# Kernel optimization log

Measured on AMD Instinct MI355X. Metric: run time of the kernel, lower is better.

## Reference

```python
import jax, jax.numpy as jnp
import numpy as np

B = 32768
DIM = 768          # emb dim
NA = 1024          # outer n_anchors
K = 8              # n_comp (= n_patches P in relays)
PD = 16            # patch_dim
RD = K * PD        # relay_dim = 128
L = 2              # n_layers (relays)
RA = 16            # anchors per patch inside RelayLayer
NPH = 3            # n_phases
TD = NPH * RA      # tri_dim = 48
H = 64             # pw_hidden
MAG_MIN, MAG_MAX = 0.1, 5.0


def _nrm(x, eps=1e-12):
    return x / jnp.maximum(jnp.linalg.norm(x, axis=-1, keepdims=True), eps)


def _ln(x, g, b, eps=1e-5):
    mu = jnp.mean(x, axis=-1, keepdims=True)
    var = jnp.mean(jnp.square(x - mu), axis=-1, keepdims=True)
    return (x - mu) * jax.lax.rsqrt(var + eps) * g + b


def setup_inputs() -> dict:
    key = jax.random.key(0)
    ks = jax.random.split(key, 16)
    xav = lambda k, shp, fan_in, fan_out: jax.random.normal(k, shp, jnp.float32) * np.sqrt(2.0 / (fan_in + fan_out))
    home = _nrm(jax.random.normal(ks[3], (L, K, RA, PD), jnp.float32))
    anchors = _nrm(home + 0.05 * jax.random.normal(ks[4], (L, K, RA, PD), jnp.float32))
    return {
        'emb': jax.random.normal(ks[0], (B, DIM), jnp.float32),
        'triangulation': jax.random.normal(ks[1], (B, NA), jnp.float32),
        'raw_magnitude': jax.random.uniform(ks[2], (B, 1), jnp.float32),
        'emb_w': xav(ks[5], (DIM, RD // 2), DIM, RD // 2), 'emb_b': jnp.zeros((RD // 2,), jnp.float32),
        'tri_w': xav(ks[6], (NA, RD // 4), NA, RD // 4), 'tri_b': jnp.zeros((RD // 4,), jnp.float32),
        'ctx_w': xav(ks[7], (RD // 2 + RD // 4 + 1, RD), RD // 2 + RD // 4 + 1, RD), 'ctx_b': jnp.zeros((RD,), jnp.float32),
        'home': home, 'anchors': anchors,
        'pw_w1': xav(ks[8], (L, K, TD, H), TD, H), 'pw_b1': jnp.zeros((L, K, H), jnp.float32),
        'pw_w2': xav(ks[9], (L, K, H, PD), H, PD), 'pw_b2': jnp.zeros((L, K, PD), jnp.float32),
        'pwn_g': jnp.ones((L, PD), jnp.float32), 'pwn_b': jnp.zeros((L, PD), jnp.float32),
        'gates': jnp.full((L, K), -3.0, jnp.float32),
        'norm_g': jnp.ones((L, RD), jnp.float32), 'norm_b': jnp.zeros((L, RD), jnp.float32),
        'head_w1': xav(ks[10], (K, PD, PD // 2), PD, PD // 2), 'head_b1': jnp.zeros((K, PD // 2), jnp.float32),
        'head_w2': xav(ks[11], (K, PD // 2, 1), PD // 2, 1), 'head_b2': jnp.zeros((K, 1), jnp.float32),
        'stats_bias': jnp.zeros((K,), jnp.float32),
    }


def _relay(x, home, anchors, w1, b1, w2, b2, pg, pb, gates, ng, nb):
    Bb = x.shape[0]
    patches = _ln(x, ng, nb).reshape(Bb, K, PD)          # [B,P,d]
    pn = _nrm(patches)
    h = _nrm(home)                                       # [P,A,d]
    c = _nrm(anchors)
    cosw = jnp.clip(jnp.sum(h * c, axis=-1), -1 + 1e-7, 1 - 1e-7)
    omega = jnp.arccos(cosw)[..., None]                  # [P,A,1]
    so = jnp.maximum(jnp.sin(omega), 1e-7)
    tris = []
    for t in (0.0, 1.0 / 3.0, 2.0 / 3.0):
        at = _nrm((jnp.sin((1.0 - t) * omega) * h + jnp.sin(t * omega) * c) / so)
        tris.append(1.0 - jnp.einsum('bpd,pad->bpa', pn, at))
    tri = jnp.concatenate(tris, axis=-1)                 # [B,P,3A]
    hh = jax.nn.gelu(jnp.einsum('bpt,pth->bph', tri, w1) + b1, approximate=False)
    pw = _ln(jnp.einsum('bph,phd->bpd', hh, w2) + b2, pg, pb)
    g = jax.nn.sigmoid(gates)[None, :, None]             # [1,P,1]
    return x + (g * pw + (1.0 - g) * patches).reshape(Bb, -1)


def reference(emb, triangulation, raw_magnitude, emb_w, emb_b, tri_w, tri_b, ctx_w, ctx_b,
              home, anchors, pw_w1, pw_b1, pw_w2, pw_b2, pwn_g, pwn_b, gates, norm_g, norm_b,
              head_w1, head_b1, head_w2, head_b2, stats_bias):
    ctx = jnp.concatenate([emb @ emb_w + emb_b, triangulation @ tri_w + tri_b, raw_magnitude], axis=-1)
    x = ctx @ ctx_w + ctx_b                              # [B, RD]
    for l in range(L):
        x = _relay(x, home[l], anchors[l], pw_w1[l], pw_b1[l], pw_w2[l], pw_b2[l],
                   pwn_g[l], pwn_b[l], gates[l], norm_g[l], norm_b[l])
    patches = x.reshape(-1, K, PD)
    h1 = jax.nn.gelu(jnp.einsum('bkd,kdh->bkh', patches, head_w1) + head_b1, approximate=False)
    mc_raw = (jnp.einsum('bkh,kho->bko', h1, head_w2) + head_b2)[..., 0]   # [B,K]
    mc = MAG_MIN + (MAG_MAX - MAG_MIN) * jax.nn.sigmoid(mc_raw + stats_bias)
    mag = jnp.repeat(mc, NA // K, axis=-1)               # [B, NA]
    return (mag, mc)
```

## Files before the change

### kernel.cpp

```cpp
#include <hip/hip_runtime.h>
#include <hip/hip_bf16.h>
#include <math.h>

#define BTOT 32768

typedef float f32x4 __attribute__((ext_vector_type(4)));
typedef __bf16 v8bf __attribute__((ext_vector_type(8)));

__device__ float g_x[BTOT * 128];
__device__ float g_M[2 * 8 * 16 * 64];
__device__ float g_b1p[2 * 8 * 64];
__device__ __align__(16) unsigned short g_wf[1792 * 128];
__device__ float g_beff[128];
__device__ float g_wr[128];

__device__ __forceinline__ float fast_rcp(float x) {
#if __has_builtin(__builtin_amdgcn_rcpf)
    return __builtin_amdgcn_rcpf(x);
#else
    return 1.f / x;
#endif
}

__device__ __forceinline__ float gelu_f(float v) {
    const float p = v * fmaf(v * v, 0.0713548162f, 1.59576912f);
    return v * fast_rcp(1.f + __expf(-p));
}

__device__ __forceinline__ float fast_sigmoid(float v) {
    return fast_rcp(1.f + __expf(-v));
}

__device__ __forceinline__ unsigned short f2bf_rne(float x) {
    unsigned u = __float_as_uint(x);
    u += 0x7fffu + ((u >> 16) & 1u);
    return (unsigned short)(u >> 16);
}

#define GLOAD16(gp, lp)                                                        \
    __builtin_amdgcn_global_load_lds(                                          \
        (const __attribute__((address_space(1))) void*)(gp),                   \
        (__attribute__((address_space(3))) void*)(lp), 16, 0, 0)

__global__ __launch_bounds__(64) void k_pre(const float* __restrict__ home,
                                            const float* __restrict__ anchors,
                                            const float* __restrict__ pw_w1,
                                            const float* __restrict__ pw_b1) {
    __shared__ float s_AT[48 * 16];
    const int lp = blockIdx.x;
    const int tid = threadIdx.x;
    if (tid < 48) {
        const int t = tid >> 4, a = tid & 15;
        const float* hp = home + (lp * 16 + a) * 16;
        const float* cp = anchors + (lp * 16 + a) * 16;
        float h[16], c[16], nh = 0.f, nc = 0.f;
#pragma unroll
        for (int i = 0; i < 16; ++i) {
            h[i] = hp[i]; nh = fmaf(h[i], h[i], nh);
            c[i] = cp[i]; nc = fmaf(c[i], c[i], nc);
        }
        const float ih = 1.f / fmaxf(sqrtf(nh), 1e-12f);
        const float ic = 1.f / fmaxf(sqrtf(nc), 1e-12f);
        float cw = 0.f;
#pragma unroll
        for (int i = 0; i < 16; ++i) { h[i] *= ih; c[i] *= ic; cw = fmaf(h[i], c[i], cw); }
        cw = fminf(fmaxf(cw, -1.f + 1e-7f), 1.f - 1e-7f);
        const float om = acosf(cw);
        const float so = fmaxf(sinf(om), 1e-7f);
        const float tt = (float)t * (1.f / 3.f);
        const float s1 = sinf((1.f - tt) * om), s2 = sinf(tt * om);
        float v[16], nv = 0.f;
#pragma unroll
        for (int i = 0; i < 16; ++i) { v[i] = (s1 * h[i] + s2 * c[i]) / so; nv = fmaf(v[i], v[i], nv); }
        const float iv = 1.f / fmaxf(sqrtf(nv), 1e-12f);
#pragma unroll
        for (int i = 0; i < 16; ++i) s_AT[tid * 16 + i] = v[i] * iv;
    }
    __syncthreads();
    const int h = tid;
    const float* w1 = pw_w1 + lp * 48 * 64;
    float b = pw_b1[lp * 64 + h];
    float m[16];
#pragma unroll
    for (int d = 0; d < 16; ++d) m[d] = 0.f;
    for (int j = 0; j < 48; ++j) {
        const float w = w1[j * 64 + h];
        b += w;
#pragma unroll
        for (int d = 0; d < 16; ++d) m[d] = fmaf(s_AT[j * 16 + d], w, m[d]);
    }
    g_b1p[lp * 64 + h] = b;
#pragma unroll
    for (int d = 0; d < 16; ++d) g_M[(lp * 16 + d) * 64 + h] = m[d];
}

__global__ __launch_bounds__(256) void k_fold(const float* __restrict__ emb_w,
                                              const float* __restrict__ tri_w,
                                              const float* __restrict__ ctx_w,
                                              const float* __restrict__ ctx_b,
                                              const float* __restrict__ emb_b,
                                              const float* __restrict__ tri_b) {
    if (blockIdx.x == 56) {
        const int n = threadIdx.x;
        if (n < 128) {
            float b = ctx_b[n];
            for (int c = 0; c < 64; ++c) b = fmaf(emb_b[c], ctx_w[c * 128 + n], b);
            for (int c = 0; c < 32; ++c) b = fmaf(tri_b[c], ctx_w[(64 + c) * 128 + n], b);
            g_beff[n] = b;
            g_wr[n] = ctx_w[96 * 128 + n];
        }
        return;
    }
    __shared__ float sctx[97 * 128];
    for (int q = threadIdx.x; q < 3104; q += 256)
        *(float4*)&sctx[q * 4] = *(const float4*)&ctx_w[q * 4];
    __syncthreads();
    const int kt = blockIdx.x;
    const int kr = threadIdx.x >> 3;
    const int n0 = (threadIdx.x & 7) * 16;
    const int k = kt * 32 + kr;
    float acc[16];
#pragma unroll
    for (int j = 0; j < 16; ++j) acc[j] = 0.f;
    if (k < 768) {
        const float* wrow = emb_w + k * 64;
        for (int c = 0; c < 64; ++c) {
            const float a = wrow[c];
            const float* cx = &sctx[c * 128 + n0];
#pragma unroll
            for (int j = 0; j < 16; ++j) acc[j] = fmaf(a, cx[j], acc[j]);
        }
    } else {
        const float* wrow = tri_w + (k - 768) * 32;
        for (int c = 0; c < 32; ++c) {
            const float a = wrow[c];
            const float* cx = &sctx[(64 + c) * 128 + n0];
#pragma unroll
            for (int j = 0; j < 16; ++j) acc[j] = fmaf(a, cx[j], acc[j]);
        }
    }
    const int nt = threadIdx.x & 7;
    const int lanehi = (kr >> 3) << 4;
    const int j8 = kr & 7;
#pragma unroll
    for (int q = 0; q < 16; ++q) {
        const int lane = lanehi | q;
        g_wf[((kt * 8 + nt) * 64 + lane) * 8 + j8] = f2bf_rne(acc[q]);
    }
}

__global__ __launch_bounds__(256) void k_front_mfma(const float* __restrict__ emb,
                                                    const float* __restrict__ tri,
                                                    const float* __restrict__ rm) {
    __shared__ __align__(16) char lds[65536];
    const int tid = threadIdx.x;
    const int lane = tid & 63, w = tid >> 6;
    const int row0 = blockIdx.x * 64;
    const int arow = lane & 15, kgrp = lane >> 4;

    f32x4 acc[8];
#pragma unroll
    for (int nt = 0; nt < 8; ++nt) {
        f32x4 z = {0.f, 0.f, 0.f, 0.f};
        acc[nt] = z;
    }

    const float* embp = emb + (size_t)(row0 + w * 16 + arow) * 768 + kgrp * 8;
    const float* trip = tri + (size_t)(row0 + w * 16 + arow) * 1024 + kgrp * 8;

    float4 A0[8], A1[8];

#define ALOAD(kk, S) {                                                         \
        const int k2_ = (kk) < 13 ? (kk) : 13;                                 \
        const float* ab_ = (k2_ < 6) ? (embp + k2_ * 128)                      \
                                     : (trip + (k2_ - 6) * 128);               \
        _Pragma("unroll")                                                      \
        for (int s = 0; s < 4; ++s) {                                          \
            S[s * 2]     = *(const float4*)(ab_ + s * 32);                     \
            S[s * 2 + 1] = *(const float4*)(ab_ + s * 32 + 4);                 \
        }                                                                      \
    }

#define STAGE_B(kk, BUF) {                                                     \
        const int k2_ = (kk) < 13 ? (kk) : 13;                                 \
        const char* gB_ = (const char*)g_wf + (size_t)k2_ * 32768              \
                          + w * 8192 + lane * 16;                              \
        char* Bb_ = lds + (BUF) * 32768 + w * 8192;               \
        _Pragma("unroll")                                                      \
        for (int i = 0; i < 8; ++i) GLOAD16(gB_ + i * 1024, Bb_ + i * 1024);   \
    }

#define COMPUTE(BUF, S) {                                                      \
        const char* Br_ = lds + (BUF) * 32768 + lane * 16;                     \
        _Pragma("unroll")                                                      \
        for (int s = 0; s < 4; ++s) {                                          \
            const float4 f0_ = S[s * 2], f1_ = S[s * 2 + 1];                   \
            v8bf a_;                                                           \
            a_[0] = (__bf16)f0_.x; a_[1] = (__bf16)f0_.y;                      \
            a_[2] = (__bf16)f0_.z; a_[3] = (__bf16)f0_.w;                      \
            a_[4] = (__bf16)f1_.x; a_[5] = (__bf16)f1_.y;                      \
            a_[6] = (__bf16)f1_.z; a_[7] = (__bf16)f1_.w;                      \
            const char* bp_ = Br_ + s * 8192;                                  \
            _Pragma("unroll")                                                  \
            for (int nt = 0; nt < 8; ++nt) {                                   \
                const v8bf b_ = *(const v8bf*)(bp_ + nt * 1024);               \
                acc[nt] = __builtin_amdgcn_mfma_f32_16x16x32_bf16(a_, b_, acc[nt], 0, 0, 0); \
            }                                                                  \
        }                                                                      \
    }

#define BODY(kk, BUFC, BUFN, SC, SN) {                                         \
        ALOAD((kk) + 1, SN);                                                   \
        STAGE_B((kk) + 1, BUFN);                                               \
        asm volatile("s_waitcnt vmcnt(16)" ::: "memory");                      \
        __builtin_amdgcn_s_barrier();                                          \
        COMPUTE(BUFC, SC);                                                     \
        __builtin_amdgcn_s_barrier();                                          \
    }

    ALOAD(0, A0);
    STAGE_B(0, 0);
    for (int t = 0; t < 6; ++t) {
        BODY(2 * t,     0, 1, A0, A1);
        BODY(2 * t + 1, 1, 0, A1, A0);
    }
    BODY(12, 0, 1, A0, A1);
    asm volatile("s_waitcnt vmcnt(0)" ::: "memory");
    __builtin_amdgcn_s_barrier();
    COMPUTE(1, A1);
#undef ALOAD
#undef STAGE_B
#undef COMPUTE
#undef BODY

    const int rowb = row0 + w * 16 + kgrp * 4;
    const f32x4 rv = *(const f32x4*)&rm[rowb];
#pragma unroll
    for (int nt = 0; nt < 8; ++nt) {
        const int col = nt * 16 + arow;
        const float be = g_beff[col];
        const float wv = g_wr[col];
#pragma unroll
        for (int rr = 0; rr < 4; ++rr) {
            g_x[(size_t)(rowb + rr) * 128 + col] = acc[nt][rr] + rv[rr] * wv + be;
        }
    }
}

__global__ __launch_bounds__(256) void k_relay(
    const float* __restrict__ pw_w2, const float* __restrict__ pw_b2,
    const float* __restrict__ pwn_g, const float* __restrict__ pwn_b,
    const float* __restrict__ gates, const float* __restrict__ norm_g,
    const float* __restrict__ norm_b, const float* __restrict__ head_w1,
    const float* __restrict__ head_b1, const float* __restrict__ head_w2,
    const float* __restrict__ head_b2, const float* __restrict__ stats_bias,
    float* __restrict__ out) {
    __shared__ __align__(16) float s_M[8 * 1028];
    __shared__ __align__(16) float s_w2[8 * 1028];
    __shared__ __align__(16) float s_b1p[8 * 68];
    __shared__ __align__(16) float s_hw1[8 * 132];
    __shared__ float s_hb1[64], s_hw2[64], s_hcb[8];
    __shared__ float s_mc[64 * 8];
    const int tid = threadIdx.x;
    const int pr = tid >> 3, p = tid & 7;
    const int rowA = blockIdx.x * 64 + pr * 2;

    {
        const int e = tid * 4, pp = e >> 7, rem = e & 127;
        *(float4*)&s_hw1[pp * 132 + rem] = *(const float4*)&head_w1[e];
    }
    if (tid < 64) { s_hb1[tid] = head_b1[tid]; s_hw2[tid] = head_w2[tid]; }
    if (tid < 8) s_hcb[tid] = head_b2[tid] + stats_bias[tid];

    float xA[16], xB[16];
    {
        const float* xp = g_x + (size_t)rowA * 128 + p * 16;
#pragma unroll
        for (int i = 0; i < 4; ++i) {
            *(float4*)&xA[i * 4] = *(const float4*)&xp[i * 4];
            *(float4*)&xB[i * 4] = *(const float4*)&xp[128 + i * 4];
        }
    }

    for (int l = 0; l < 2; ++l) {
        if (l) __syncthreads();
        for (int q = tid; q < 2048; q += 256) {
            const int e = q * 4, pp = e >> 10, rem = e & 1023;
            *(float4*)&s_M[pp * 1028 + rem] = *(const float4*)&g_M[l * 8192 + e];
            *(float4*)&s_w2[pp * 1028 + rem] = *(const float4*)&pw_w2[l * 8192 + e];
        }
        if (tid < 128) {
            const int e = tid * 4, pp = e >> 6, rem = e & 63;
            *(float4*)&s_b1p[pp * 68 + rem] = *(const float4*)&g_b1p[l * 512 + e];
        }
        __syncthreads();

        float sA = 0.f, qA = 0.f, sB = 0.f, qB = 0.f;
#pragma unroll
        for (int i = 0; i < 16; ++i) {
            sA += xA[i]; qA = fmaf(xA[i], xA[i], qA);
            sB += xB[i]; qB = fmaf(xB[i], xB[i], qB);
        }
#pragma unroll
        for (int m = 1; m < 8; m <<= 1) {
            sA += __shfl_xor(sA, m, 64); qA += __shfl_xor(qA, m, 64);
            sB += __shfl_xor(sB, m, 64); qB += __shfl_xor(qB, m, 64);
        }
        const float muA = sA * (1.f / 128.f);
        const float rsA = rsqrtf(fmaxf(qA * (1.f / 128.f) - muA * muA, 0.f) + 1e-5f);
        const float muB = sB * (1.f / 128.f);
        const float rsB = rsqrtf(fmaxf(qB * (1.f / 128.f) - muB * muB, 0.f) + 1e-5f);
        float paA[16], paB[16], nA = 0.f, nB = 0.f;
#pragma unroll
        for (int i = 0; i < 16; ++i) {
            const float gg = norm_g[l * 128 + p * 16 + i];
            const float bb = norm_b[l * 128 + p * 16 + i];
            const float vA = (xA[i] - muA) * rsA * gg + bb;
            const float vB = (xB[i] - muB) * rsB * gg + bb;
            paA[i] = vA; nA = fmaf(vA, vA, nA);
            paB[i] = vB; nB = fmaf(vB, vB, nB);
        }
        const float invA = 1.f / fmaxf(sqrtf(nA), 1e-12f);
        const float invB = 1.f / fmaxf(sqrtf(nB), 1e-12f);

        float pwA[16], pwB[16];
#pragma unroll
        for (int i = 0; i < 16; ++i) {
            const float b2 = pw_b2[(l * 8 + p) * 16 + i];
            pwA[i] = b2; pwB[i] = b2;
        }
        const float* Mp = &s_M[p * 1028];
        const float* W2p = &s_w2[p * 1028];
        const float* Bp = &s_b1p[p * 68];
        for (int h4 = 0; h4 < 16; ++h4) {
            float bq[4];
            *(float4*)bq = *(const float4*)&Bp[h4 * 4];
            float aA[4] = {0.f, 0.f, 0.f, 0.f};
            float aB[4] = {0.f, 0.f, 0.f, 0.f};
#pragma unroll
            for (int d = 0; d < 16; ++d) {
                float m4[4];
                *(float4*)m4 = *(const float4*)&Mp[d * 64 + h4 * 4];
#pragma unroll
                for (int j = 0; j < 4; ++j) {
                    aA[j] = fmaf(paA[d], m4[j], aA[j]);
                    aB[j] = fmaf(paB[d], m4[j], aB[j]);
                }
            }
#pragma unroll
            for (int j = 0; j < 4; ++j) {
                const float gA = gelu_f(bq[j] - invA * aA[j]);
                const float gB = gelu_f(bq[j] - invB * aB[j]);
                float w[16];
#pragma unroll
                for (int u = 0; u < 4; ++u)
                    *(float4*)&w[u * 4] = *(const float4*)&W2p[(h4 * 4 + j) * 16 + u * 4];
#pragma unroll
                for (int u = 0; u < 16; ++u) {
                    pwA[u] = fmaf(gA, w[u], pwA[u]);
                    pwB[u] = fmaf(gB, w[u], pwB[u]);
                }
            }
        }
        float s2A = 0.f, q2A = 0.f, s2B = 0.f, q2B = 0.f;
#pragma unroll
        for (int i = 0; i < 16; ++i) {
            s2A += pwA[i]; q2A = fmaf(pwA[i], pwA[i], q2A);
            s2B += pwB[i]; q2B = fmaf(pwB[i], pwB[i], q2B);
        }
        const float mu2A = s2A * (1.f / 16.f);
        const float rs2A = rsqrtf(fmaxf(q2A * (1.f / 16.f) - mu2A * mu2A, 0.f) + 1e-5f);
        const float mu2B = s2B * (1.f / 16.f);
        const float rs2B = rsqrtf(fmaxf(q2B * (1.f / 16.f) - mu2B * mu2B, 0.f) + 1e-5f);
        const float gate = fast_sigmoid(gates[l * 8 + p]);
#pragma unroll
        for (int i = 0; i < 16; ++i) {
            const float pg = pwn_g[l * 16 + i], pb = pwn_b[l * 16 + i];
            const float vA = (pwA[i] - mu2A) * rs2A * pg + pb;
            const float vB = (pwB[i] - mu2B) * rs2B * pg + pb;
            xA[i] = xA[i] + gate * vA + (1.f - gate) * paA[i];
            xB[i] = xB[i] + gate * vB + (1.f - gate) * paB[i];
        }
    }

    float accmA = s_hcb[p], accmB = accmA;
#pragma unroll
    for (int j = 0; j < 8; ++j) {
        float aA = s_hb1[p * 8 + j], aB = aA;
#pragma unroll
        for (int d = 0; d < 16; ++d) {
            const float w = s_hw1[p * 132 + d * 8 + j];
            aA = fmaf(xA[d], w, aA);
            aB = fmaf(xB[d], w, aB);
        }
        const float w2h = s_hw2[p * 8 + j];
        accmA = fmaf(gelu_f(aA), w2h, accmA);
        accmB = fmaf(gelu_f(aB), w2h, accmB);
    }
    const float mcA = 0.1f + 4.9f * fast_sigmoid(accmA);
    const float mcB = 0.1f + 4.9f * fast_sigmoid(accmB);
    s_mc[(pr * 2) * 8 + p] = mcA;
    s_mc[(pr * 2 + 1) * 8 + p] = mcB;
    out[(size_t)33554432 + (size_t)rowA * 8 + p] = mcA;
    out[(size_t)33554432 + (size_t)(rowA + 1) * 8 + p] = mcB;
    __syncthreads();

    const size_t base = (size_t)blockIdx.x * 64 * 1024;
#pragma unroll
    for (int it = 0; it < 64; ++it) {
        const int idx = it * 256 + tid;
        const int rr = idx >> 8, c4 = idx & 255;
        const float v = s_mc[rr * 8 + (c4 >> 5)];
        const float4 vv = make_float4(v, v, v, v);
        *(float4*)&out[base + rr * 1024 + c4 * 4] = vv;
    }
}

extern "C" void kernel_launch(void* const* d_in, const int* in_sizes, int n_in,
                              void* d_out, int out_size, void* d_ws, size_t ws_size,
                              hipStream_t stream) {
    (void)in_sizes; (void)n_in; (void)d_ws; (void)ws_size; (void)out_size;
    const float* emb = (const float*)d_in[0];
    const float* tria = (const float*)d_in[1];
    const float* rm = (const float*)d_in[2];
    const float* emb_w = (const float*)d_in[3];
    const float* emb_b = (const float*)d_in[4];
    const float* tri_w = (const float*)d_in[5];
    const float* tri_b = (const float*)d_in[6];
    const float* ctx_w = (const float*)d_in[7];
    const float* ctx_b = (const float*)d_in[8];
    const float* home = (const float*)d_in[9];
    const float* anch = (const float*)d_in[10];
    const float* pw_w1 = (const float*)d_in[11];
    const float* pw_b1 = (const float*)d_in[12];
    const float* pw_w2 = (const float*)d_in[13];
    const float* pw_b2 = (const float*)d_in[14];
    const float* pwn_g = (const float*)d_in[15];
    const float* pwn_b = (const float*)d_in[16];
    const float* gates = (const float*)d_in[17];
    const float* norm_g = (const float*)d_in[18];
    const float* norm_b = (const float*)d_in[19];
    const float* hw1 = (const float*)d_in[20];
    const float* hb1 = (const float*)d_in[21];
    const float* hw2 = (const float*)d_in[22];
    const float* hb2 = (const float*)d_in[23];
    const float* sb = (const float*)d_in[24];
    float* out = (float*)d_out;

    k_pre<<<16, 64, 0, stream>>>(home, anch, pw_w1, pw_b1);
    k_fold<<<57, 256, 0, stream>>>(emb_w, tri_w, ctx_w, ctx_b, emb_b, tri_b);
    k_front_mfma<<<512, 256, 0, stream>>>(emb, tria, rm);
    k_relay<<<512, 256, 0, stream>>>(pw_w2, pw_b2, pwn_g, pwn_b, gates, norm_g, norm_b,
                                     hw1, hb1, hw2, hb2, sb, out);
}
```

Baseline: 161.0 us.

## Shrink front GEMM blocks to 32 rows with 64-wide K stages

The front MFMA GEMM now runs 128-thread blocks of 32 rows each with 1024 blocks, and uses 64-wide K chunks (28 stages) instead of 128-wide ones, halving LDS to 32KB. It also replaces the manual vmcnt-based pipeline with a plain double buffer using __syncthreads. The aim is higher occupancy and more blocks per CU. In exchange the weight tile is reloaded by twice as many blocks, and there are more barriers per unit of work.

```diff
diff --git a/kernel.cpp b/kernel.cpp
--- a/kernel.cpp
+++ b/kernel.cpp
@@ -149,13 +149,13 @@
     }
 }
 
-__global__ __launch_bounds__(256) void k_front_mfma(const float* __restrict__ emb,
+__global__ __launch_bounds__(128) void k_front_mfma(const float* __restrict__ emb,
                                                     const float* __restrict__ tri,
                                                     const float* __restrict__ rm) {
-    __shared__ __align__(16) char lds[65536];
+    __shared__ __align__(16) char lds[32768];
     const int tid = threadIdx.x;
     const int lane = tid & 63, w = tid >> 6;
-    const int row0 = blockIdx.x * 64;
+    const int row0 = blockIdx.x * 32;
     const int arow = lane & 15, kgrp = lane >> 4;
 
     f32x4 acc[8];
@@ -168,39 +168,36 @@
     const float* embp = emb + (size_t)(row0 + w * 16 + arow) * 768 + kgrp * 8;
     const float* trip = tri + (size_t)(row0 + w * 16 + arow) * 1024 + kgrp * 8;
 
-    float4 A0[8], A1[8];
+    float4 A0[4], A1[4];
 
 #define ALOAD(kk, S) {                                                         \
-        const int k2_ = (kk) < 13 ? (kk) : 13;                                 \
-        const float* ab_ = (k2_ < 6) ? (embp + k2_ * 128)                      \
-                                     : (trip + (k2_ - 6) * 128);               \
-        _Pragma("unroll")                                                      \
-        for (int s = 0; s < 4; ++s) {                                          \
-            S[s * 2]     = *(const float4*)(ab_ + s * 32);                     \
-            S[s * 2 + 1] = *(const float4*)(ab_ + s * 32 + 4);                 \
-        }                                                                      \
+        const float* ab_ = ((kk) < 12) ? (embp + (kk) * 64)                    \
+                                       : (trip + ((kk) - 12) * 64);            \
+        S[0] = *(const float4*)(ab_);                                          \
+        S[1] = *(const float4*)(ab_ + 4);                                      \
+        S[2] = *(const float4*)(ab_ + 32);                                     \
+        S[3] = *(const float4*)(ab_ + 36);                                     \
     }
 
 #define STAGE_B(kk, BUF) {                                                     \
-        const int k2_ = (kk) < 13 ? (kk) : 13;                                 \
-        const char* gB_ = (const char*)g_wf + (size_t)k2_ * 32768              \
+        const char* gB_ = (const char*)g_wf + (size_t)(kk) * 16384             \
                           + w * 8192 + lane * 16;                              \
-        char* Bb_ = lds + (BUF) * 32768 + w * 8192;               \
+        char* Bb_ = lds + (BUF) * 16384 + w * 8192;               \
         _Pragma("unroll")                                                      \
         for (int i = 0; i < 8; ++i) GLOAD16(gB_ + i * 1024, Bb_ + i * 1024);   \
     }
 
 #define COMPUTE(BUF, S) {                                                      \
-        const char* Br_ = lds + (BUF) * 32768 + lane * 16;                     \
+        const char* Br_ = lds + (BUF) * 16384 + lane * 16;                     \
         _Pragma("unroll")                                                      \
-        for (int s = 0; s < 4; ++s) {                                          \
-            const float4 f0_ = S[s * 2], f1_ = S[s * 2 + 1];                   \
+        for (int h = 0; h < 2; ++h) {                                          \
+            const float4 f0_ = S[h * 2], f1_ = S[h * 2 + 1];                   \
             v8bf a_;                                                           \
             a_[0] = (__bf16)f0_.x; a_[1] = (__bf16)f0_.y;                      \
             a_[2] = (__bf16)f0_.z; a_[3] = (__bf16)f0_.w;                      \
             a_[4] = (__bf16)f1_.x; a_[5] = (__bf16)f1_.y;                      \
             a_[6] = (__bf16)f1_.z; a_[7] = (__bf16)f1_.w;                      \
-            const char* bp_ = Br_ + s * 8192;                                  \
+            const char* bp_ = Br_ + h * 8192;                                  \
             _Pragma("unroll")                                                  \
             for (int nt = 0; nt < 8; ++nt) {                                   \
                 const v8bf b_ = *(const v8bf*)(bp_ + nt * 1024);               \
@@ -209,29 +206,24 @@
         }                                                                      \
     }
 
-#define BODY(kk, BUFC, BUFN, SC, SN) {                                         \
-        ALOAD((kk) + 1, SN);                                                   \
-        STAGE_B((kk) + 1, BUFN);                                               \
-        asm volatile("s_waitcnt vmcnt(16)" ::: "memory");                      \
-        __builtin_amdgcn_s_barrier();                                          \
-        COMPUTE(BUFC, SC);                                                     \
-        __builtin_amdgcn_s_barrier();                                          \
-    }
-
     ALOAD(0, A0);
     STAGE_B(0, 0);
-    for (int t = 0; t < 6; ++t) {
-        BODY(2 * t,     0, 1, A0, A1);
-        BODY(2 * t + 1, 1, 0, A1, A0);
-    }
-    BODY(12, 0, 1, A0, A1);
-    asm volatile("s_waitcnt vmcnt(0)" ::: "memory");
-    __builtin_amdgcn_s_barrier();
-    COMPUTE(1, A1);
+    __syncthreads();
+    for (int t = 0; t < 14; ++t) {
+        ALOAD(2 * t + 1, A1);
+        STAGE_B(2 * t + 1, 1);
+        COMPUTE(0, A0);
+        __syncthreads();
+        if (t < 13) {
+            ALOAD(2 * t + 2, A0);
+            STAGE_B(2 * t + 2, 0);
+        }
+        COMPUTE(1, A1);
+        __syncthreads();
+    }
 #undef ALOAD
 #undef STAGE_B
 #undef COMPUTE
-#undef BODY
 
     const int rowb = row0 + w * 16 + kgrp * 4;
     const f32x4 rv = *(const f32x4*)&rm[rowb];
@@ -449,7 +441,7 @@
 
     k_pre<<<16, 64, 0, stream>>>(home, anch, pw_w1, pw_b1);
     k_fold<<<57, 256, 0, stream>>>(emb_w, tri_w, ctx_w, ctx_b, emb_b, tri_b);
-    k_front_mfma<<<512, 256, 0, stream>>>(emb, tria, rm);
+    k_front_mfma<<<1024, 128, 0, stream>>>(emb, tria, rm);
     k_relay<<<512, 256, 0, stream>>>(pw_w2, pw_b2, pwn_g, pwn_b, gates, norm_g, norm_b,
                                      hw1, hb1, hw2, hb2, sb, out);
 }
```

Measured after the change: 174.6 us. 1.08x slower.
